# Kernel optimization log

Hardware: AMD Instinct MI355X
Metric: run time of the kernel (lower is better)

Reference implementation:

```python
import jax, jax.numpy as jnp
import numpy as np

B = 2_000_000
_SHIFTS = jnp.arange(31, -1, -1, dtype=jnp.uint32)  # MSB-first bit order


def _float_to_bits(f):
    """f32 [...] -> pulse bits [..., 32] in {0.,1.}, MSB first."""
    u = jax.lax.bitcast_convert_type(f.astype(jnp.float32), jnp.uint32)
    return ((u[..., None] >> _SHIFTS) & jnp.uint32(1)).astype(jnp.float32)


def _bits_to_float(bits):
    """pulse bits [..., 32] -> f32 [...]."""
    b = (bits > 0.5).astype(jnp.uint32)
    u = jnp.sum(b << _SHIFTS, axis=-1, dtype=jnp.uint32)
    return jax.lax.bitcast_convert_type(u, jnp.float32)


def setup_inputs() -> dict:
    key = jax.random.key(0)
    vals = jax.random.normal(key, (B,), dtype=jnp.float32) * 3.0
    return {"x": _float_to_bits(vals)}


def reference(x):
    # SpikeFP32Sigmoid: flip sign bit -> exp -> 1 + exp(-x) -> 1 / (1 + exp(-x)).
    # The gate circuit implements exact FP32 arithmetic on the bit-pulses, so the
    # equivalent math is: decode bits -> sigmoid in fp32 -> re-encode bits.
    f = _bits_to_float(x)              # [B]
    s = jax.nn.sigmoid(f)              # 1 / (1 + exp(-f)) in fp32
    return _float_to_bits(s)           # [B, 32]
```

## Files before the change

### kernel.cpp

```cpp
#include <hip/hip_runtime.h>

__device__ __forceinline__ float xla_expf(float xin) {
#pragma clang fp contract(off)
  float xc = fminf(xin, 88.3762626647950f);
  xc = fmaxf(xc, -88.3762626647949f);
  float m = floorf(fmaf(xc, 1.44269504088896341f, 0.5f));
  float r = fmaf(m, -0.693359375f, xc);
  r = fmaf(m, 2.12194440e-4f, r);
  float r2 = r * r;
  float y = 1.9875691500E-4f;
  y = fmaf(y, r, 1.3981999507E-3f);
  y = fmaf(y, r, 8.3334519073E-3f);
  y = fmaf(y, r, 4.1665795894E-2f);
  y = fmaf(y, r, 1.6666665459E-1f);
  y = fmaf(y, r, 5.0000001201E-1f);
  y = fmaf(y, r2, r);
  y = y + 1.0f;
  int n = (int)m;
  float twon = __int_as_float((n + 127) << 23);
  float res = y * twon;
  return fmaxf(res, xin);
}

__device__ __forceinline__ float xla_sigmoid(float f) {
#pragma clang fp contract(off)
  float e = xla_expf(-f);
  float denom = 1.0f + e;
  return 1.0f / denom;
}

#define KSEG 8

__global__ void __launch_bounds__(256) spike_sigmoid_kernel(
    const float* __restrict__ in, float* __restrict__ out, int nseg) {
  int W = (blockIdx.x * 256 + threadIdx.x) >> 6;
  int lane = threadIdx.x & 63;
  int seg0 = W * KSEG;
  if (seg0 >= nseg) return;
  size_t base = (size_t)seg0 * 64 + lane;
  int sel = lane >> 5;
  int bitpos = 31 - (lane & 31);
  int srcbase = sel * 4;

  if (seg0 + KSEG <= nseg) {
    float f[KSEG];
#pragma unroll
    for (int k = 0; k < KSEG; ++k) f[k] = in[base + (size_t)k * 64];

    unsigned u[16];
#pragma unroll
    for (int k = 0; k < KSEG; ++k) {
      unsigned long long b = __ballot(f[k] > 0.5f);
      u[2 * k]     = __brev((unsigned)b);
      u[2 * k + 1] = __brev((unsigned)(b >> 32));
    }

    bool p2 = (lane >> 2) & 1, p3 = (lane >> 3) & 1;
    bool p4 = (lane >> 4) & 1, p5 = (lane >> 5) & 1;
    unsigned a0 = p2 ? u[1]  : u[0],  a1 = p2 ? u[3]  : u[2];
    unsigned a2 = p2 ? u[5]  : u[4],  a3 = p2 ? u[7]  : u[6];
    unsigned a4 = p2 ? u[9]  : u[8],  a5 = p2 ? u[11] : u[10];
    unsigned a6 = p2 ? u[13] : u[12], a7 = p2 ? u[15] : u[14];
    unsigned b0 = p3 ? a1 : a0, b1 = p3 ? a3 : a2;
    unsigned b2 = p3 ? a5 : a4, b3 = p3 ? a7 : a6;
    unsigned c0 = p4 ? b1 : b0, c1 = p4 ? b3 : b2;
    unsigned v  = p5 ? c1 : c0;

    float s = xla_sigmoid(__uint_as_float(v));
    unsigned sb = __float_as_uint(s);

#pragma unroll
    for (int k = 0; k < KSEG; ++k) {
      unsigned x = (unsigned)__shfl((int)sb, 8 * k + srcbase);
      float o = (float)((x >> bitpos) & 1u);
      __builtin_nontemporal_store(o, &out[base + (size_t)k * 64]);
    }
  } else {
    for (int k = 0; k < KSEG && seg0 + k < nseg; ++k) {
      float fk = in[base + (size_t)k * 64];
      unsigned long long b = __ballot(fk > 0.5f);
      unsigned u0 = __brev((unsigned)b);
      unsigned u1 = __brev((unsigned)(b >> 32));
      unsigned uu = sel ? u1 : u0;
      float s = xla_sigmoid(__uint_as_float(uu));
      unsigned sb = __float_as_uint(s);
      float o = (float)((sb >> bitpos) & 1u);
      __builtin_nontemporal_store(o, &out[base + (size_t)k * 64]);
    }
  }
}

extern "C" void kernel_launch(void* const* d_in, const int* in_sizes, int n_in,
                              void* d_out, int out_size, void* d_ws, size_t ws_size,
                              hipStream_t stream) {
  const float* in = (const float*)d_in[0];
  float* out = (float*)d_out;
  int nseg = in_sizes[0] / 64;
  int waves = (nseg + KSEG - 1) / KSEG;
  long long threads = (long long)waves * 64;
  dim3 block(256);
  dim3 grid((unsigned)((threads + 255) / 256));
  spike_sigmoid_kernel<<<grid, block, 0, stream>>>(in, out, nseg);
}
```

Baseline: 75.14 us.

## Convert to persistent grid-stride kernel with next-iteration load prefetch

Measured after the change: 79.60 us. 1.06x slower.

```diff
diff --git a/kernel.cpp b/kernel.cpp
--- a/kernel.cpp
+++ b/kernel.cpp
@@ -33,21 +33,35 @@
 
 __global__ void __launch_bounds__(256) spike_sigmoid_kernel(
     const float* __restrict__ in, float* __restrict__ out, int nseg) {
-  int W = (blockIdx.x * 256 + threadIdx.x) >> 6;
+  int gw = (blockIdx.x * 256 + threadIdx.x) >> 6;
+  int nw = (gridDim.x * 256) >> 6;
   int lane = threadIdx.x & 63;
-  int seg0 = W * KSEG;
-  if (seg0 >= nseg) return;
-  size_t base = (size_t)seg0 * 64 + lane;
   int sel = lane >> 5;
   int bitpos = 31 - (lane & 31);
   int srcbase = sel * 4;
+  bool p2 = (lane >> 2) & 1, p3 = (lane >> 3) & 1;
+  bool p4 = (lane >> 4) & 1, p5 = (lane >> 5) & 1;
 
-  if (seg0 + KSEG <= nseg) {
-    float f[KSEG];
+  int s = gw * KSEG;
+  int stride = nw * KSEG;
+  if (s >= nseg) return;
+
+  size_t base = (size_t)s * 64 + lane;
+  float f[KSEG];
 #pragma unroll
-    for (int k = 0; k < KSEG; ++k) f[k] = in[base + (size_t)k * 64];
+  for (int k = 0; k < KSEG; ++k) f[k] = in[base + (size_t)k * 64];
 
-    unsigned u[16];
+  while (true) {
+    int snext = s + stride;
+    size_t nbase = (size_t)snext * 64 + lane;
+    float fn[KSEG];
+    bool have = snext < nseg;
+    if (have) {
+#pragma unroll
+      for (int k = 0; k < KSEG; ++k) fn[k] = in[nbase + (size_t)k * 64];
+    }
+
+    unsigned u[2 * KSEG];
 #pragma unroll
     for (int k = 0; k < KSEG; ++k) {
       unsigned long long b = __ballot(f[k] > 0.5f);
@@ -55,8 +69,6 @@
       u[2 * k + 1] = __brev((unsigned)(b >> 32));
     }
 
-    bool p2 = (lane >> 2) & 1, p3 = (lane >> 3) & 1;
-    bool p4 = (lane >> 4) & 1, p5 = (lane >> 5) & 1;
     unsigned a0 = p2 ? u[1]  : u[0],  a1 = p2 ? u[3]  : u[2];
     unsigned a2 = p2 ? u[5]  : u[4],  a3 = p2 ? u[7]  : u[6];
     unsigned a4 = p2 ? u[9]  : u[8],  a5 = p2 ? u[11] : u[10];
@@ -66,8 +78,8 @@
     unsigned c0 = p4 ? b1 : b0, c1 = p4 ? b3 : b2;
     unsigned v  = p5 ? c1 : c0;
 
-    float s = xla_sigmoid(__uint_as_float(v));
-    unsigned sb = __float_as_uint(s);
+    float sg = xla_sigmoid(__uint_as_float(v));
+    unsigned sb = __float_as_uint(sg);
 
 #pragma unroll
     for (int k = 0; k < KSEG; ++k) {
@@ -75,18 +87,12 @@
       float o = (float)((x >> bitpos) & 1u);
       __builtin_nontemporal_store(o, &out[base + (size_t)k * 64]);
     }
-  } else {
-    for (int k = 0; k < KSEG && seg0 + k < nseg; ++k) {
-      float fk = in[base + (size_t)k * 64];
-      unsigned long long b = __ballot(fk > 0.5f);
-      unsigned u0 = __brev((unsigned)b);
-      unsigned u1 = __brev((unsigned)(b >> 32));
-      unsigned uu = sel ? u1 : u0;
-      float s = xla_sigmoid(__uint_as_float(uu));
-      unsigned sb = __float_as_uint(s);
-      float o = (float)((sb >> bitpos) & 1u);
-      __builtin_nontemporal_store(o, &out[base + (size_t)k * 64]);
-    }
+
+    if (!have) break;
+    s = snext;
+    base = nbase;
+#pragma unroll
+    for (int k = 0; k < KSEG; ++k) f[k] = fn[k];
   }
 }
 
@@ -96,9 +102,7 @@
   const float* in = (const float*)d_in[0];
   float* out = (float*)d_out;
   int nseg = in_sizes[0] / 64;
-  int waves = (nseg + KSEG - 1) / KSEG;
-  long long threads = (long long)waves * 64;
   dim3 block(256);
-  dim3 grid((unsigned)((threads + 255) / 256));
+  dim3 grid(2048);
   spike_sigmoid_kernel<<<grid, block, 0, stream>>>(in, out, nseg);
 }
```
